# Kernel optimization log

Hardware: AMD Instinct MI355X
Metric: run time of the kernel (lower is better)

The kernel has to match this reference:

```python
import jax, jax.numpy as jnp
import numpy as np

B, T, D, H = 4, 2048, 1024, 16
HD = D // H
SCALE = D ** (-0.5)  # note: module scales by d_model**-0.5, not head_dim**-0.5


def setup_inputs() -> dict:
    key = jax.random.key(0)
    k1, k2, k3 = jax.random.split(key, 3)
    x = jax.random.normal(k1, (B, T, D), dtype=jnp.float32)
    Wqkv = jax.random.normal(k2, (D, 3 * D), dtype=jnp.float32) * (D ** -0.5)
    Wo = jax.random.normal(k3, (D, D), dtype=jnp.float32) * (D ** -0.5)
    return {"x": x, "Wqkv": Wqkv, "Wo": Wo}


def reference(x, Wqkv, Wo):
    b, t, c = x.shape
    qkv = x @ Wqkv  # [B,T,3D]
    q, k, v = jnp.split(qkv, 3, axis=-1)
    q = q.reshape(b, t, H, HD).transpose(0, 2, 1, 3)  # [B,H,T,HD]
    k = k.reshape(b, t, H, HD).transpose(0, 2, 1, 3)
    v = v.reshape(b, t, H, HD).transpose(0, 2, 1, 3)
    attn = jnp.einsum('bhid,bhjd->bhij', q, k) * SCALE  # [B,H,T,T]
    mask = jnp.tril(jnp.ones((t, t), dtype=jnp.bool_))
    attn = jnp.where(mask[None, None], attn, jnp.finfo(attn.dtype).min)
    attn = jax.nn.softmax(attn, axis=-1)
    out = jnp.einsum('bhij,bhjd->bhid', attn, v)  # [B,H,T,HD]
    out = out.transpose(0, 2, 1, 3).reshape(b, t, c)
    return out @ Wo
```

## Files before the change

kernel.cpp:

```cpp
#include <hip/hip_runtime.h>
#include <hip/hip_bf16.h>

#define B_ 4
#define T_ 2048
#define D_ 1024
#define H_ 16
#define HD_ 64

typedef __bf16 bf16;
typedef __bf16 bf16x8 __attribute__((ext_vector_type(8)));
typedef __bf16 bf16x4 __attribute__((ext_vector_type(4)));
typedef float f32x4 __attribute__((ext_vector_type(4)));
typedef float f32x16 __attribute__((ext_vector_type(16)));

#define MFMA16(a, b, c) __builtin_amdgcn_mfma_f32_16x16x32_bf16(a, b, c, 0, 0, 0)
#define MFMA32(a, b, c) __builtin_amdgcn_mfma_f32_32x32x16_bf16(a, b, c, 0, 0, 0)

__device__ inline void gld_lds16(const bf16* g, bf16* l) {
  __builtin_amdgcn_global_load_lds((const __attribute__((address_space(1))) void*)g,
                                   (__attribute__((address_space(3))) void*)l, 16, 0, 0);
}

__device__ inline unsigned pkbf16(float a, float b) {
  unsigned r;
  asm("v_cvt_pk_bf16_f32 %0, %1, %2" : "=v"(r) : "v"(a), "v"(b));
  return r;
}
__device__ inline void pl32swap(unsigned& x, unsigned& y) {
  asm("v_permlane32_swap_b32 %0, %1" : "+v"(x), "+v"(y));
}

#define PACKJ(dst, S, base)                        \
  {                                                \
    unsigned w0 = pkbf16(S[base + 0], S[base + 1]); \
    unsigned w2 = pkbf16(S[base + 4], S[base + 5]); \
    pl32swap(w0, w2);                              \
    unsigned w1 = pkbf16(S[base + 2], S[base + 3]); \
    unsigned w3 = pkbf16(S[base + 6], S[base + 7]); \
    pl32swap(w1, w3);                              \
    int4 wi = {(int)w0, (int)w1, (int)w2, (int)w3}; \
    dst = __builtin_bit_cast(bf16x8, wi);          \
  }

__global__ void cvt_f32_bf16(const float* __restrict__ in, bf16* __restrict__ out) {
  int i = (blockIdx.x * 256 + threadIdx.x) * 4;
  float4 v = *(const float4*)(in + i);
  bf16x4 o = {(bf16)v.x, (bf16)v.y, (bf16)v.z, (bf16)v.w};
  *(bf16x4*)(out + i) = o;
}

__global__ void transpose_f32_bf16(const float* __restrict__ in, bf16* __restrict__ out,
                                   int R, int C) {
  __shared__ float tile[32][33];
  int c0 = blockIdx.x * 32, r0 = blockIdx.y * 32;
  int tx = threadIdx.x, ty = threadIdx.y;
#pragma unroll
  for (int i = 0; i < 4; i++)
    tile[ty + i * 8][tx] = in[(size_t)(r0 + ty + i * 8) * C + c0 + tx];
  __syncthreads();
#pragma unroll
  for (int i = 0; i < 4; i++)
    out[(size_t)(c0 + ty + i * 8) * R + r0 + tx] = (bf16)tile[tx][ty + i * 8];
}

__global__ void transpose_v(const bf16* __restrict__ in, bf16* __restrict__ out) {
  __shared__ bf16 tile[32][33];
  int bh = blockIdx.y;
  int t0 = blockIdx.x * 32;
  int tx = threadIdx.x, ty = threadIdx.y;
  const bf16* ib = in + (size_t)bh * T_ * HD_;
  bf16* ob = out + (size_t)bh * HD_ * T_;
#pragma unroll
  for (int d0 = 0; d0 < 64; d0 += 32) {
#pragma unroll
    for (int i = 0; i < 4; i++)
      tile[ty + i * 8][tx] = ib[(size_t)(t0 + ty + i * 8) * HD_ + d0 + tx];
    __syncthreads();
#pragma unroll
    for (int i = 0; i < 4; i++)
      ob[(size_t)(d0 + ty + i * 8) * T_ + t0 + tx] = tile[tx][ty + i * 8];
    __syncthreads();
  }
}

template <int EPI>
__global__ __launch_bounds__(256) void gemm_bt(const bf16* __restrict__ A,
                                               const bf16* __restrict__ Bt,
                                               bf16* __restrict__ qb, bf16* __restrict__ kb,
                                               bf16* __restrict__ vb, float* __restrict__ fout,
                                               int M, int N, int K) {
  __shared__ __align__(16) bf16 lds_a[3][128 * 32];
  __shared__ __align__(16) bf16 lds_b[3][128 * 32];
  int n0 = blockIdx.x * 128, m0 = blockIdx.y * 128;
  int tid = threadIdx.x, wave = tid >> 6, lane = tid & 63;
  int l16 = lane & 15, lhi = lane >> 4;
  int wr = wave >> 1, wc = wave & 1;
  f32x4 acc[4][4];
#pragma unroll
  for (int mt = 0; mt < 4; mt++)
#pragma unroll
    for (int nt = 0; nt < 4; nt++) acc[mt][nt] = (f32x4){0.f, 0.f, 0.f, 0.f};

  int sr = wave * 16 + (lane >> 2);
  int scol = (lane & 3) * 8;
  const bf16* ga = A + (size_t)(m0 + sr) * K + scol;
  const bf16* gb = Bt + (size_t)(n0 + sr) * K + scol;

  auto STAGE = [&](int buf, int k0) {
    gld_lds16(ga + k0, &lds_a[buf][wave * 512]);
    gld_lds16(ga + (size_t)64 * K + k0, &lds_a[buf][2048 + wave * 512]);
    gld_lds16(gb + k0, &lds_b[buf][wave * 512]);
    gld_lds16(gb + (size_t)64 * K + k0, &lds_b[buf][2048 + wave * 512]);
  };

  int NT = K >> 5;
  STAGE(0, 0);
  STAGE(1, 32);
  int cur = 0, nx = 2;
  for (int t = 0; t < NT; t++) {
    if (t + 1 < NT)
      asm volatile("s_waitcnt vmcnt(4)" ::: "memory");
    else
      asm volatile("s_waitcnt vmcnt(0)" ::: "memory");
    __builtin_amdgcn_s_barrier();
    if (t + 2 < NT) STAGE(nx, (t + 2) * 32);
    const bf16* la = lds_a[cur];
    const bf16* lb = lds_b[cur];
    bf16x8 af[4], bfr[4];
#pragma unroll
    for (int mt = 0; mt < 4; mt++)
      af[mt] = *(const bf16x8*)&la[(wr * 64 + mt * 16 + l16) * 32 + 8 * lhi];
#pragma unroll
    for (int nt = 0; nt < 4; nt++)
      bfr[nt] = *(const bf16x8*)&lb[(wc * 64 + nt * 16 + l16) * 32 + 8 * lhi];
    __builtin_amdgcn_s_setprio(1);
#pragma unroll
    for (int mt = 0; mt < 4; mt++)
#pragma unroll
      for (int nt = 0; nt < 4; nt++) acc[mt][nt] = MFMA16(af[mt], bfr[nt], acc[mt][nt]);
    __builtin_amdgcn_s_setprio(0);
    cur = (cur == 2) ? 0 : cur + 1;
    nx = (nx == 2) ? 0 : nx + 1;
  }

#pragma unroll
  for (int mt = 0; mt < 4; mt++)
#pragma unroll
    for (int nt = 0; nt < 4; nt++)
#pragma unroll
      for (int rr = 0; rr < 4; rr++) {
        int row = m0 + wr * 64 + mt * 16 + 4 * lhi + rr;
        int col = n0 + wc * 64 + nt * 16 + l16;
        float v = acc[mt][nt][rr];
        if (EPI == 0) {
          int b = row >> 11, t = row & (T_ - 1);
          int sec = col >> 10, c2 = col & 1023;
          int h = c2 >> 6, d = c2 & 63;
          size_t idx = ((size_t)(b * H_ + h) * T_ + t) * HD_ + d;
          if (sec == 0)
            qb[idx] = (bf16)(v * 0.045084439f);
          else if (sec == 1)
            kb[idx] = (bf16)v;
          else
            vb[idx] = (bf16)v;
        } else {
          fout[(size_t)row * N + col] = v;
        }
      }
}

__global__ __launch_bounds__(256) void attn_kernel(const bf16* __restrict__ qbuf,
                                                   const bf16* __restrict__ kbuf,
                                                   const bf16* __restrict__ vtbuf,
                                                   bf16* __restrict__ obuf) {
  __shared__ __align__(16) bf16 sm[24576];
  int bid = blockIdx.x;
  int bh = (bid & 7) * 8 + ((bid >> 3) & 7);
  const int qtab[16] = {15, 14, 13, 12, 8, 9, 10, 11, 6, 4, 5, 7, 1, 3, 2, 0};
  int qi = qtab[bid >> 6];
  int q0 = qi * 128;
  int wv = threadIdx.x >> 6;
  int lane = threadIdx.x & 63;
  int q = lane & 31, hi = lane >> 5;
  int qw = q0 + wv * 32;
  int b = bh >> 4, h = bh & 15;

  const bf16* Q = qbuf + (size_t)bh * T_ * HD_;
  const bf16* Kg = kbuf + (size_t)bh * T_ * HD_;
  const bf16* Vt = vtbuf + (size_t)bh * HD_ * T_;

  bf16x8 qf[4];
#pragma unroll
  for (int j = 0; j < 4; j++)
    qf[j] = *(const bf16x8*)(Q + (size_t)(qw + q) * HD_ + j * 16 + hi * 8);

  int srow = lane >> 3;
  int sc8 = ((lane & 7) ^ srow) * 8;
  int r0 = wv * 16;
  const bf16* kgp = Kg + (size_t)(r0 + srow) * HD_ + sc8;
  const bf16* vgp = Vt + (size_t)(r0 + srow) * T_ + sc8;

  auto stage = [&](int buf, int t) {
    const bf16* kg = kgp + (size_t)t * 64 * HD_;
    const bf16* vg = vgp + t * 64;
    bf16* kd = sm + buf * 4096;
    bf16* vd = sm + 12288 + buf * 4096;
    gld_lds16(kg, kd + r0 * 64);
    gld_lds16(kg + 8 * HD_, kd + (r0 + 8) * 64);
    gld_lds16(vg, vd + r0 * 64);
    gld_lds16(vg + 8 * T_, vd + (r0 + 8) * 64);
  };

  int xo = (q & 7) << 4;
  int A0 = q * 128 + ((16 * hi) ^ xo);
  int A1 = q * 128 + ((32 + 16 * hi) ^ xo);
  int A2 = q * 128 + ((64 + 16 * hi) ^ xo);
  int A3 = q * 128 + ((96 + 16 * hi) ^ xo);
  const char* smc = (const char*)sm;

  f32x16 o1, o2;
#pragma unroll
  for (int r = 0; r < 16; r++) {
    o1[r] = 0.f;
    o2[r] = 0.f;
  }
  float m_r = -1e30f, l_r = 0.f;
  int ntm = 2 * qi + 2;

  auto compute = [&](int KB, int t) {
    int jb = t * 64;
    if (jb > qw + 31) return;
    int VB = KB + 24576;
    bf16x8 kf[8];
    kf[0] = *(const bf16x8*)(smc + KB + A0);
    kf[1] = *(const bf16x8*)(smc + KB + A1);
    kf[2] = *(const bf16x8*)(smc + KB + A2);
    kf[3] = *(const bf16x8*)(smc + KB + A3);
    kf[4] = *(const bf16x8*)(smc + KB + 4096 + A0);
    kf[5] = *(const bf16x8*)(smc + KB + 4096 + A1);
    kf[6] = *(const bf16x8*)(smc + KB + 4096 + A2);
    kf[7] = *(const bf16x8*)(smc + KB + 4096 + A3);
    f32x16 s1, s2;
#pragma unroll
    for (int r = 0; r < 16; r++) {
      s1[r] = 0.f;
      s2[r] = 0.f;
    }
    __builtin_amdgcn_s_setprio(1);
#pragma unroll
    for (int j = 0; j < 4; j++) s1 = MFMA32(kf[j], qf[j], s1);
#pragma unroll
    for (int j = 0; j < 4; j++) s2 = MFMA32(kf[4 + j], qf[j], s2);
    __builtin_amdgcn_s_setprio(0);
    if (jb + 63 > qw) {
#pragma unroll
      for (int r = 0; r < 16; r++) {
        int kv = (r & 3) + 8 * (r >> 2) + 4 * hi;
        if (jb + kv > qw + q) s1[r] = -1e30f;
        if (jb + kv + 32 > qw + q) s2[r] = -1e30f;
      }
    }
    float tm[8];
#pragma unroll
    for (int r = 0; r < 8; r++)
      tm[r] = fmaxf(fmaxf(s1[r], s1[r + 8]), fmaxf(s2[r], s2[r + 8]));
#pragma unroll
    for (int r = 0; r < 4; r++) tm[r] = fmaxf(tm[r], tm[r + 4]);
    float mx = fmaxf(fmaxf(tm[0], tm[1]), fmaxf(tm[2], tm[3]));
    mx = fmaxf(mx, __shfl_xor(mx, 32));
    bool defer = __all(mx <= m_r + 8.f);
    if (!defer) {
      float mn = fmaxf(m_r, mx);
      float sc = exp2f(m_r - mn);
      m_r = mn;
      l_r *= sc;
#pragma unroll
      for (int r = 0; r < 16; r++) {
        o1[r] *= sc;
        o2[r] *= sc;
      }
    }
#pragma unroll
    for (int r = 0; r < 16; r++) s1[r] = exp2f(s1[r] - m_r);
#pragma unroll
    for (int r = 0; r < 16; r++) s2[r] = exp2f(s2[r] - m_r);
    float ts[8];
#pragma unroll
    for (int r = 0; r < 8; r++) ts[r] = (s1[r] + s1[r + 8]) + (s2[r] + s2[r + 8]);
#pragma unroll
    for (int r = 0; r < 4; r++) ts[r] += ts[r + 4];
    float su = (ts[0] + ts[1]) + (ts[2] + ts[3]);
    su += __shfl_xor(su, 32);
    l_r += su;
    bf16x8 pf0, pf1, pf2, pf3;
    PACKJ(pf0, s1, 0);
    PACKJ(pf1, s1, 8);
    PACKJ(pf2, s2, 0);
    PACKJ(pf3, s2, 8);
    bf16x8 vf[8];
    vf[0] = *(const bf16x8*)(smc + VB + A0);
    vf[1] = *(const bf16x8*)(smc + VB + A1);
    vf[2] = *(const bf16x8*)(smc + VB + A2);
    vf[3] = *(const bf16x8*)(smc + VB + A3);
    vf[4] = *(const bf16x8*)(smc + VB + 4096 + A0);
    vf[5] = *(const bf16x8*)(smc + VB + 4096 + A1);
    vf[6] = *(const bf16x8*)(smc + VB + 4096 + A2);
    vf[7] = *(const bf16x8*)(smc + VB + 4096 + A3);
    __builtin_amdgcn_s_setprio(1);
    o1 = MFMA32(vf[0], pf0, o1);
    o2 = MFMA32(vf[4], pf0, o2);
    o1 = MFMA32(vf[1], pf1, o1);
    o2 = MFMA32(vf[5], pf1, o2);
    o1 = MFMA32(vf[2], pf2, o1);
    o2 = MFMA32(vf[6], pf2, o2);
    o1 = MFMA32(vf[3], pf3, o1);
    o2 = MFMA32(vf[7], pf3, o2);
    __builtin_amdgcn_s_setprio(0);
  };

  stage(0, 0);
  stage(1, 1);
  int cur = 0, nx = 2;
  for (int t = 0; t < ntm; ++t) {
    if (t + 1 < ntm)
      asm volatile("s_waitcnt vmcnt(4)" ::: "memory");
    else
      asm volatile("s_waitcnt vmcnt(0)" ::: "memory");
    __builtin_amdgcn_s_barrier();
    if (t + 2 < ntm) stage(nx, t + 2);
    compute(cur * 8192, t);
    cur = (cur == 2) ? 0 : cur + 1;
    nx = (nx == 2) ? 0 : nx + 1;
  }
  __syncthreads();

  bf16* scr = sm + wv * 2112;
  float inv = 1.f / l_r;
#pragma unroll
  for (int r = 0; r < 16; r++) {
    int d = (r & 3) + 8 * (r >> 2) + 4 * hi;
    scr[d * 33 + q] = (bf16)(o1[r] * inv);
    scr[(32 + d) * 33 + q] = (bf16)(o2[r] * inv);
  }
#pragma unroll
  for (int pass = 0; pass < 4; pass++) {
    int row = qw + pass * 8 + (lane >> 3);
    int dcol = (lane & 7) * 8;
    bf16x8 ov;
#pragma unroll
    for (int e = 0; e < 8; e++) ov[e] = scr[(dcol + e) * 33 + pass * 8 + (lane >> 3)];
    *(bf16x8*)(obuf + ((size_t)(b * T_ + row)) * D_ + h * 64 + dcol) = ov;
  }
}

extern "C" void kernel_launch(void* const* d_in, const int* in_sizes, int n_in, void* d_out,
                              int out_size, void* d_ws, size_t ws_size, hipStream_t stream) {
  const float* x = (const float*)d_in[0];
  const float* wqkv = (const float*)d_in[1];
  const float* wo = (const float*)d_in[2];
  float* out = (float*)d_out;
  char* ws = (char*)d_ws;

  bf16* xb = (bf16*)ws;
  bf16* wqkvt = (bf16*)(ws + (16u << 20));
  bf16* wot = (bf16*)(ws + (22u << 20));
  bf16* qb = (bf16*)(ws + (24u << 20));
  bf16* kb = (bf16*)(ws + (40u << 20));
  bf16* vb = (bf16*)(ws + (56u << 20));
  bf16* vtb = (bf16*)(ws + (72u << 20));
  bf16* ao = (bf16*)(ws + (88u << 20));

  cvt_f32_bf16<<<8192, 256, 0, stream>>>(x, xb);
  transpose_f32_bf16<<<dim3(96, 32), dim3(32, 8), 0, stream>>>(wqkv, wqkvt, 1024, 3072);
  transpose_f32_bf16<<<dim3(32, 32), dim3(32, 8), 0, stream>>>(wo, wot, 1024, 1024);
  gemm_bt<0><<<dim3(24, 64), 256, 0, stream>>>(xb, wqkvt, qb, kb, vb, nullptr,
                                               B_ * T_, 3 * D_, D_);
  transpose_v<<<dim3(64, 64), dim3(32, 8), 0, stream>>>(vb, vtb);
  attn_kernel<<<1024, 256, 0, stream>>>(qb, kb, vtb, ao);
  gemm_bt<1><<<dim3(8, 64), 256, 0, stream>>>(ao, wot, nullptr, nullptr, nullptr, out,
                                              B_ * T_, D_, D_);
}
```

Before: 197.7 us.

## Load V fragments directly from global memory and shrink K pipeline to double buffer

V tiles are no longer staged through LDS. Each wave reads its V^T fragments straight from global memory into registers at the start of each compute step, and the K ring buffer drops from three stages to two with a plain __syncthreads per iteration. LDS use falls, which may raise occupancy. The cost is that the V global loads now sit exposed on the critical path, with uncoalesced strided reads and no async prefetch depth, and the full barrier per iteration replaces the finer vmcnt-based waits.

```diff
diff --git a/kernel.cpp b/kernel.cpp
--- a/kernel.cpp
+++ b/kernel.cpp
@@ -173,7 +173,7 @@
                                                    const bf16* __restrict__ kbuf,
                                                    const bf16* __restrict__ vtbuf,
                                                    bf16* __restrict__ obuf) {
-  __shared__ __align__(16) bf16 sm[24576];
+  __shared__ __align__(16) bf16 sm[8704];
   int bid = blockIdx.x;
   int bh = (bid & 7) * 8 + ((bid >> 3) & 7);
   const int qtab[16] = {15, 14, 13, 12, 8, 9, 10, 11, 6, 4, 5, 7, 1, 3, 2, 0};
@@ -198,18 +198,15 @@
   int sc8 = ((lane & 7) ^ srow) * 8;
   int r0 = wv * 16;
   const bf16* kgp = Kg + (size_t)(r0 + srow) * HD_ + sc8;
-  const bf16* vgp = Vt + (size_t)(r0 + srow) * T_ + sc8;
 
   auto stage = [&](int buf, int t) {
     const bf16* kg = kgp + (size_t)t * 64 * HD_;
-    const bf16* vg = vgp + t * 64;
     bf16* kd = sm + buf * 4096;
-    bf16* vd = sm + 12288 + buf * 4096;
     gld_lds16(kg, kd + r0 * 64);
     gld_lds16(kg + 8 * HD_, kd + (r0 + 8) * 64);
-    gld_lds16(vg, vd + r0 * 64);
-    gld_lds16(vg + 8 * T_, vd + (r0 + 8) * 64);
   };
+
+  const bf16* vbase = Vt + (size_t)q * T_ + hi * 8;
 
   int xo = (q & 7) << 4;
   int A0 = q * 128 + ((16 * hi) ^ xo);
@@ -230,7 +227,12 @@
   auto compute = [&](int KB, int t) {
     int jb = t * 64;
     if (jb > qw + 31) return;
-    int VB = KB + 24576;
+    bf16x8 vf[8];
+#pragma unroll
+    for (int j = 0; j < 4; j++) {
+      vf[j] = *(const bf16x8*)(vbase + jb + j * 16);
+      vf[4 + j] = *(const bf16x8*)(vbase + 32 * T_ + jb + j * 16);
+    }
     bf16x8 kf[8];
     kf[0] = *(const bf16x8*)(smc + KB + A0);
     kf[1] = *(const bf16x8*)(smc + KB + A1);
@@ -297,15 +299,6 @@
     PACKJ(pf1, s1, 8);
     PACKJ(pf2, s2, 0);
     PACKJ(pf3, s2, 8);
-    bf16x8 vf[8];
-    vf[0] = *(const bf16x8*)(smc + VB + A0);
-    vf[1] = *(const bf16x8*)(smc + VB + A1);
-    vf[2] = *(const bf16x8*)(smc + VB + A2);
-    vf[3] = *(const bf16x8*)(smc + VB + A3);
-    vf[4] = *(const bf16x8*)(smc + VB + 4096 + A0);
-    vf[5] = *(const bf16x8*)(smc + VB + 4096 + A1);
-    vf[6] = *(const bf16x8*)(smc + VB + 4096 + A2);
-    vf[7] = *(const bf16x8*)(smc + VB + 4096 + A3);
     __builtin_amdgcn_s_setprio(1);
     o1 = MFMA32(vf[0], pf0, o1);
     o2 = MFMA32(vf[4], pf0, o2);
@@ -319,20 +312,12 @@
   };
 
   stage(0, 0);
-  stage(1, 1);
-  int cur = 0, nx = 2;
+  __syncthreads();
   for (int t = 0; t < ntm; ++t) {
-    if (t + 1 < ntm)
-      asm volatile("s_waitcnt vmcnt(4)" ::: "memory");
-    else
-      asm volatile("s_waitcnt vmcnt(0)" ::: "memory");
-    __builtin_amdgcn_s_barrier();
-    if (t + 2 < ntm) stage(nx, t + 2);
-    compute(cur * 8192, t);
-    cur = (cur == 2) ? 0 : cur + 1;
-    nx = (nx == 2) ? 0 : nx + 1;
-  }
-  __syncthreads();
+    if (t + 1 < ntm) stage((t + 1) & 1, t + 1);
+    compute((t & 1) * 8192, t);
+    __syncthreads();
+  }
 
   bf16* scr = sm + wv * 2112;
   float inv = 1.f / l_r;
```

New measurement: 211.8 us. 7.1% more time.
